# Kernel optimization log

Measured on AMD Instinct MI355X. Metric: run time of the kernel, lower is better.

## Reference

```python
import jax, jax.numpy as jnp
import numpy as np

B, NA, T, NV, D = 24, 50, 10, 196, 512


def setup_inputs() -> dict:
    key = jax.random.key(0)
    k1, k2 = jax.random.split(key)
    return {
        "audio_feats": jax.random.normal(k1, (B, NA, D), dtype=jnp.float32),
        "visual_feats": jax.random.normal(k2, (B, T, NV, D), dtype=jnp.float32),
        "temperature": jnp.float32(2.5),
        "scale_factor": jnp.float32(2.5),
        "threshold": jnp.float32(-2.5),
    }


def _l2norm(x):
    # F.normalize(dim=-1): x / max(||x||, 1e-12)
    n = jnp.sqrt(jnp.sum(x * x, axis=-1, keepdims=True))
    return x / jnp.maximum(n, 1e-12)


def reference(audio_feats, visual_feats, temperature, scale_factor, threshold):
    b = audio_feats.shape[0]
    a = _l2norm(audio_feats)          # (B,Na,D)
    v = _l2norm(visual_feats)         # (B,T,Nv,D)
    # all-pairs token similarities: (B,B,Na,T,Nv)
    sims = jnp.einsum('xad,ytvd->xyatv', a, v) / temperature

    # aggregate_temporal_similarities
    th = jax.nn.sigmoid(threshold)
    max_vis = jnp.max(sims, axis=-1)            # (B,B,Na,T)
    raw_diff = max_vis - th
    sel = jax.nn.relu(raw_diff) * scale_factor  # selection strength
    weighted_sum = jnp.sum(max_vis * sel, axis=-1)   # over T
    weights_sum = jnp.sum(sel, axis=-1)
    token_sims = weighted_sum / jnp.maximum(weights_sum, 1e-6)
    clip_sims = jnp.mean(token_sims, axis=-1)   # (B,B)
    fraction_selected = jnp.mean((raw_diff > 0).astype(jnp.float32))

    # InfoNCE
    idx = jnp.arange(b)
    losses_a2v = -jax.nn.log_softmax(clip_sims, axis=1)[idx, idx]
    losses_v2a = -jax.nn.log_softmax(clip_sims.T, axis=1)[idx, idx]
    contrastive_loss = jnp.mean(losses_a2v + losses_v2a) / 2

    # regularization
    neg = jnp.clip(sims, -20.0, 0.0)
    l_nonneg = jnp.mean(neg * neg)
    temp_low = jnp.maximum(-jnp.log(temperature), 0.0) ** 2   # log(1)=0
    temp_high = jnp.maximum(jnp.log(temperature) - jnp.log(4.0), 0.0) ** 2
    l_cal = temp_low + temp_high
    l_threshold = jnp.maximum(th - 0.9, 0.0) ** 2 + jnp.maximum(0.1 - th, 0.0) ** 2
    l_scale = jnp.maximum(scale_factor - 20.0, 0.0) ** 2 + jnp.maximum(1.0 - scale_factor, 0.0) ** 2
    reg_loss = 0.15 * l_nonneg + 2.0 * l_cal + 0.1 * l_threshold + 0.1 * l_scale

    # selection reward on positive pairs (diagonal)
    pos_diffs = raw_diff[idx, idx]                       # (B,Na,T)
    sel_ratio = (jnp.tanh(20.0 * pos_diffs) + 1.0) / 2.0
    selection_reward = -0.1 * jnp.log1p(jnp.mean(sel_ratio))

    total_loss = selection_reward + contrastive_loss + reg_loss
    return (total_loss, contrastive_loss, reg_loss, fraction_selected, selection_reward)
```

## Files before the change

kernel.cpp:

```cpp
#include <hip/hip_runtime.h>
#include <math.h>

#define B_   24
#define NA_  50
#define T_   10
#define NV_  196
#define D_   512
#define M_   1200
#define MPAD 1280
#define NVP  224
#define YT_  240
#define VROWS (YT_ * NVP)
#define ABLK 320

typedef __bf16 bf16x8 __attribute__((ext_vector_type(8)));
typedef float  f32x4  __attribute__((ext_vector_type(4)));
typedef unsigned short ushort8 __attribute__((ext_vector_type(8)));

__device__ __forceinline__ unsigned short f2bf(float f) {
    unsigned u = __float_as_uint(f);
    u += 0x7FFF + ((u >> 16) & 1);
    return (unsigned short)(u >> 16);
}

__device__ __forceinline__ void gload16(const void* g, void* l) {
    __builtin_amdgcn_global_load_lds(
        (const __attribute__((address_space(1))) unsigned int*)g,
        (__attribute__((address_space(3))) unsigned int*)l, 16, 0, 0);
}

__global__ void normconv_kernel(const float* __restrict__ a,
                                const float* __restrict__ vf,
                                const float* __restrict__ tempPtr,
                                unsigned short* __restrict__ Abf,
                                unsigned short* __restrict__ Vbf,
                                float* __restrict__ accs) {
    if (blockIdx.x == 0 && threadIdx.x < 4) accs[threadIdx.x] = 0.0f;
    int w = threadIdx.x >> 6, lane = threadIdx.x & 63;
    int bid = blockIdx.x;
    const float* src = nullptr;
    ushort8* dst;
    float tscale = 1.0f;
    if (bid < ABLK) {
        int row = bid * 4 + w;
        dst = (ushort8*)(Abf + (size_t)row * D_ + lane * 8);
        if (row < M_) { src = a + (size_t)row * D_ + lane * 8; tscale = tempPtr[0]; }
    } else {
        int row = (bid - ABLK) * 4 + w;
        dst = (ushort8*)(Vbf + (size_t)row * D_ + lane * 8);
        int yt = row / NVP, vv = row - yt * NVP;
        if (vv < NV_) src = vf + ((size_t)yt * NV_ + vv) * D_ + lane * 8;
    }
    if (src) {
        float4 u = *(const float4*)src;
        float4 v = *(const float4*)(src + 4);
        float s = u.x*u.x + u.y*u.y + u.z*u.z + u.w*u.w
                + v.x*v.x + v.y*v.y + v.z*v.z + v.w*v.w;
        #pragma unroll
        for (int off = 32; off; off >>= 1) s += __shfl_xor(s, off, 64);
        float sc = 1.0f / (fmaxf(sqrtf(s), 1e-12f) * tscale);
        ushort8 o;
        o[0]=f2bf(u.x*sc); o[1]=f2bf(u.y*sc); o[2]=f2bf(u.z*sc); o[3]=f2bf(u.w*sc);
        o[4]=f2bf(v.x*sc); o[5]=f2bf(v.y*sc); o[6]=f2bf(v.z*sc); o[7]=f2bf(v.w*sc);
        *dst = o;
    } else {
        ushort8 z = (ushort8)0;
        *dst = z;
    }
}

__global__ __launch_bounds__(256) void simred_kernel(
    const unsigned short* __restrict__ Abf, const unsigned short* __restrict__ Vbf,
    float* __restrict__ maxvis, float* __restrict__ accNonneg)
{
    __shared__ __align__(16) unsigned char lds[8192 + 14336];
    __shared__ float maxred[2][128];
    __shared__ float redbuf[4];

    const int tid  = threadIdx.x;
    const int lane = tid & 63;
    const int w    = tid >> 6;
    const int lrow = lane >> 2;
    const int lcol = lane & 3;
    const int q    = lane >> 4;
    const int m16  = lane & 15;
    const int wr   = w & 1;
    const int wc   = w >> 1;

    const int lin = blockIdx.y * gridDim.x + blockIdx.x;
    const int swz = (lin & 7) * 300 + (lin >> 3);
    const int bx  = swz % 10;
    const int yt  = swz / 10;
    const int rowA0 = bx * 128;
    const size_t vRow0 = (size_t)yt * NVP;

    const int scol = lcol ^ ((lrow >> 1) & 3);
    const unsigned short* gp[6];
    const unsigned char*  lp[6];
    int nun = 0;
    for (int u = w; u < 22; u += 4) {
        if (u < 8) gp[nun] = Abf + ((size_t)(rowA0 + u * 16 + lrow)) * D_ + scol * 8;
        else       gp[nun] = Vbf + (vRow0 + (size_t)((u - 8) * 16 + lrow)) * D_ + scol * 8;
        lp[nun] = lds + u * 1024;
        ++nun;
    }

    const unsigned rsw = (unsigned)((m16 >> 1) & 3) * 16u;
    unsigned aoff[4], boff[7];
    #pragma unroll
    for (int i = 0; i < 4; ++i)
        aoff[i] = (unsigned)(wr * 64 + i * 16 + m16) * 64u + (((unsigned)q * 16u) ^ rsw);
    #pragma unroll
    for (int j = 0; j < 7; ++j)
        boff[j] = 8192u + (unsigned)(wc * 112 + j * 16 + m16) * 64u + (((unsigned)q * 16u) ^ rsw);

    f32x4 acc[4][7];
    #pragma unroll
    for (int i = 0; i < 4; ++i)
        #pragma unroll
        for (int j = 0; j < 7; ++j) acc[i][j] = (f32x4)0.0f;

    #pragma unroll 6
    for (int i = 0; i < 6; ++i)
        if (i < nun) gload16(gp[i], (void*)lp[i]);
    __syncthreads();

    for (int c = 0; c < 16; ++c) {
        bf16x8 af[4], bfr[7];
        #pragma unroll
        for (int i = 0; i < 4; ++i) af[i] = *(const bf16x8*)(lds + aoff[i]);
        #pragma unroll
        for (int j = 0; j < 7; ++j) bfr[j] = *(const bf16x8*)(lds + boff[j]);
        __syncthreads();
        if (c < 15) {
            const int kc2 = (c + 1) * 32;
            #pragma unroll 6
            for (int i = 0; i < 6; ++i)
                if (i < nun) gload16(gp[i] + kc2, (void*)lp[i]);
        }
        #pragma unroll
        for (int i = 0; i < 4; ++i)
            #pragma unroll
            for (int j = 0; j < 7; ++j)
                acc[i][j] = __builtin_amdgcn_mfma_f32_16x16x32_bf16(af[i], bfr[j], acc[i][j], 0, 0, 0);
        __syncthreads();
    }

    float cs = 0.0f;
    #pragma unroll
    for (int i = 0; i < 4; ++i)
        #pragma unroll
        for (int j = 0; j < 7; ++j)
            #pragma unroll
            for (int r = 0; r < 4; ++r) {
                float v = acc[i][j][r];
                float cv = fminf(fmaxf(v, -20.0f), 0.0f);
                cs += cv * cv;
            }
    #pragma unroll
    for (int off = 32; off; off >>= 1) cs += __shfl_xor(cs, off, 64);
    if (lane == 0) redbuf[w] = cs;

    bool colv[7];
    #pragma unroll
    for (int j = 0; j < 7; ++j) colv[j] = (wc * 112 + j * 16 + m16) < NV_;
    #pragma unroll
    for (int i = 0; i < 4; ++i) {
        float mx[4] = {-3e38f, -3e38f, -3e38f, -3e38f};
        #pragma unroll
        for (int j = 0; j < 7; ++j)
            #pragma unroll
            for (int r = 0; r < 4; ++r)
                mx[r] = fmaxf(mx[r], colv[j] ? acc[i][j][r] : -3e38f);
        #pragma unroll
        for (int r = 0; r < 4; ++r) {
            float mm = mx[r];
            #pragma unroll
            for (int off = 1; off <= 8; off <<= 1) mm = fmaxf(mm, __shfl_xor(mm, off, 64));
            if (m16 == 0) maxred[wc][wr * 64 + i * 16 + q * 4 + r] = mm;
        }
    }
    __syncthreads();
    if (tid == 0) atomicAdd(accNonneg, redbuf[0] + redbuf[1] + redbuf[2] + redbuf[3]);
    if (tid < 128) {
        float mm = fmaxf(maxred[0][tid], maxred[1][tid]);
        int R = rowA0 + tid;
        if (R < M_) {
            int x = R / NA_, a = R - x * NA_;
            int y = yt / T_, t = yt - y * T_;
            maxvis[(((size_t)x * B_ + y) * NA_ + a) * T_ + t] = mm;
        }
    }
}

__global__ void aggfin_kernel(const float* __restrict__ maxvis,
                              const float* __restrict__ thrPtr,
                              const float* __restrict__ scalePtr,
                              const float* __restrict__ tempPtr,
                              float* __restrict__ clipSims,
                              float* __restrict__ accs,
                              float* __restrict__ out)
{
    int xy = blockIdx.x;
    int x = xy / B_, y = xy % B_;
    int a = threadIdx.x;
    float th    = 1.0f / (1.0f + expf(-thrPtr[0]));
    float scale = scalePtr[0];
    float token = 0.0f, cnt = 0.0f, selsum = 0.0f;
    if (a < NA_) {
        const float* p = maxvis + (((size_t)x * B_ + y) * NA_ + a) * T_;
        float ws = 0.0f, ss = 0.0f;
        #pragma unroll
        for (int t = 0; t < T_; ++t) {
            float mv  = p[t];
            float rd  = mv - th;
            float sel = fmaxf(rd, 0.0f) * scale;
            ws += mv * sel;
            ss += sel;
            if (rd > 0.0f) cnt += 1.0f;
            if (x == y) selsum += 0.5f * (tanhf(20.0f * rd) + 1.0f);
        }
        token = ws / fmaxf(ss, 1e-6f);
    }
    #pragma unroll
    for (int off = 32; off; off >>= 1) {
        token  += __shfl_xor(token,  off, 64);
        cnt    += __shfl_xor(cnt,    off, 64);
        selsum += __shfl_xor(selsum, off, 64);
    }
    if (threadIdx.x == 0) {
        clipSims[x * B_ + y] = token / (float)NA_;
        atomicAdd(&accs[1], cnt);
        if (x == y) atomicAdd(&accs[2], selsum);
    }
    __threadfence();
    unsigned last = 0;
    if (threadIdx.x == 0) {
        unsigned v = atomicAdd((unsigned int*)(accs + 3), 1u);
        last = ((v % (unsigned)(B_ * B_)) == (unsigned)(B_ * B_ - 1));
    }
    last = __shfl((int)last, 0, 64);
    if (!last) return;
    __threadfence();

    __shared__ float cs[B_ * B_];
    int tid = threadIdx.x;
    for (int i = tid; i < B_ * B_; i += 64) cs[i] = clipSims[i];
    __syncthreads();
    float lsum = 0.0f;
    if (tid < B_) {
        int i = tid;
        float m = -1e30f;
        for (int j = 0; j < B_; ++j) m = fmaxf(m, cs[i * B_ + j]);
        float e = 0.0f;
        for (int j = 0; j < B_; ++j) e += expf(cs[i * B_ + j] - m);
        float la = m + logf(e) - cs[i * B_ + i];
        float m2 = -1e30f;
        for (int j = 0; j < B_; ++j) m2 = fmaxf(m2, cs[j * B_ + i]);
        float e2 = 0.0f;
        for (int j = 0; j < B_; ++j) e2 += expf(cs[j * B_ + i] - m2);
        float lv = m2 + logf(e2) - cs[i * B_ + i];
        lsum = la + lv;
    }
    #pragma unroll
    for (int off = 32; off; off >>= 1) lsum += __shfl_xor(lsum, off, 64);
    if (tid == 0) {
        float contrastive = lsum / (float)B_ * 0.5f;
        float temp = tempPtr[0], scl = scalePtr[0];
        float l_nonneg = accs[0] / 56448000.0f;
        float logt = logf(temp);
        float tl  = fmaxf(-logt, 0.0f);
        float thi = fmaxf(logt - logf(4.0f), 0.0f);
        float l_cal = tl * tl + thi * thi;
        float t1 = fmaxf(th - 0.9f, 0.0f), t2 = fmaxf(0.1f - th, 0.0f);
        float l_thr = t1 * t1 + t2 * t2;
        float s1 = fmaxf(scl - 20.0f, 0.0f), s2 = fmaxf(1.0f - scl, 0.0f);
        float l_scale = s1 * s1 + s2 * s2;
        float reg = 0.15f * l_nonneg + 2.0f * l_cal + 0.1f * l_thr + 0.1f * l_scale;
        float frac   = accs[1] / 288000.0f;
        float selrew = -0.1f * log1pf(accs[2] / 12000.0f);
        out[0] = selrew + contrastive + reg;
        out[1] = contrastive;
        out[2] = reg;
        out[3] = frac;
        out[4] = selrew;
    }
}

extern "C" void kernel_launch(void* const* d_in, const int* in_sizes, int n_in,
                              void* d_out, int out_size, void* d_ws, size_t ws_size,
                              hipStream_t stream) {
    const float* audio  = (const float*)d_in[0];
    const float* visual = (const float*)d_in[1];
    const float* temp   = (const float*)d_in[2];
    const float* scale  = (const float*)d_in[3];
    const float* thr    = (const float*)d_in[4];
    float* out = (float*)d_out;

    unsigned char* wsb = (unsigned char*)d_ws;
    unsigned short* Abf = (unsigned short*)wsb;
    unsigned short* Vbf = (unsigned short*)(wsb + 1310720);
    float* maxvis   = (float*)(wsb + 1310720 + 55050240);
    float* clipSims = (float*)(wsb + 1310720 + 55050240 + 1152000);
    float* accs     = clipSims + 576;

    normconv_kernel<<<ABLK + VROWS / 4, 256, 0, stream>>>(audio, visual, temp, Abf, Vbf, accs);

    dim3 grid(MPAD / 128, YT_);
    simred_kernel<<<grid, 256, 0, stream>>>(Abf, Vbf, maxvis, accs);

    aggfin_kernel<<<B_ * B_, 64, 0, stream>>>(maxvis, thr, scale, temp, clipSims, accs, out);
}
```

Before: 285.9 us.

## Load MFMA operands directly from global memory instead of staging through LDS

Removes the LDS staging buffer and the global_load_lds double-step, so each wave reads its bf16 A and V fragments straight from global memory (via cache) inside a fully unrolled K loop, with no barriers. It also sets launch bounds to allow two blocks per CU. This trades the LDS writes and reads and the per-iteration syncs for redundant global/L2 traffic, since fragments shared across waves are now fetched separately by each wave. The operands also lose cooperative coalesced loading.

Result: slower. 408.7 us (+42.9%).

```diff
diff --git a/kernel.cpp b/kernel.cpp
--- a/kernel.cpp
+++ b/kernel.cpp
@@ -21,12 +21,6 @@
     unsigned u = __float_as_uint(f);
     u += 0x7FFF + ((u >> 16) & 1);
     return (unsigned short)(u >> 16);
-}
-
-__device__ __forceinline__ void gload16(const void* g, void* l) {
-    __builtin_amdgcn_global_load_lds(
-        (const __attribute__((address_space(1))) unsigned int*)g,
-        (__attribute__((address_space(3))) unsigned int*)l, 16, 0, 0);
 }
 
 __global__ void normconv_kernel(const float* __restrict__ a,
@@ -69,19 +63,16 @@
     }
 }
 
-__global__ __launch_bounds__(256) void simred_kernel(
+__global__ __launch_bounds__(256, 2) void simred_kernel(
     const unsigned short* __restrict__ Abf, const unsigned short* __restrict__ Vbf,
     float* __restrict__ maxvis, float* __restrict__ accNonneg)
 {
-    __shared__ __align__(16) unsigned char lds[8192 + 14336];
     __shared__ float maxred[2][128];
     __shared__ float redbuf[4];
 
     const int tid  = threadIdx.x;
     const int lane = tid & 63;
     const int w    = tid >> 6;
-    const int lrow = lane >> 2;
-    const int lcol = lane & 3;
     const int q    = lane >> 4;
     const int m16  = lane & 15;
     const int wr   = w & 1;
@@ -94,25 +85,14 @@
     const int rowA0 = bx * 128;
     const size_t vRow0 = (size_t)yt * NVP;
 
-    const int scol = lcol ^ ((lrow >> 1) & 3);
-    const unsigned short* gp[6];
-    const unsigned char*  lp[6];
-    int nun = 0;
-    for (int u = w; u < 22; u += 4) {
-        if (u < 8) gp[nun] = Abf + ((size_t)(rowA0 + u * 16 + lrow)) * D_ + scol * 8;
-        else       gp[nun] = Vbf + (vRow0 + (size_t)((u - 8) * 16 + lrow)) * D_ + scol * 8;
-        lp[nun] = lds + u * 1024;
-        ++nun;
-    }
-
-    const unsigned rsw = (unsigned)((m16 >> 1) & 3) * 16u;
-    unsigned aoff[4], boff[7];
+    const unsigned short* pA[4];
+    const unsigned short* pB[7];
     #pragma unroll
     for (int i = 0; i < 4; ++i)
-        aoff[i] = (unsigned)(wr * 64 + i * 16 + m16) * 64u + (((unsigned)q * 16u) ^ rsw);
+        pA[i] = Abf + ((size_t)(rowA0 + wr * 64 + i * 16 + m16)) * D_ + q * 8;
     #pragma unroll
     for (int j = 0; j < 7; ++j)
-        boff[j] = 8192u + (unsigned)(wc * 112 + j * 16 + m16) * 64u + (((unsigned)q * 16u) ^ rsw);
+        pB[j] = Vbf + (vRow0 + (size_t)(wc * 112 + j * 16 + m16)) * D_ + q * 8;
 
     f32x4 acc[4][7];
     #pragma unroll
@@ -120,30 +100,18 @@
         #pragma unroll
         for (int j = 0; j < 7; ++j) acc[i][j] = (f32x4)0.0f;
 
-    #pragma unroll 6
-    for (int i = 0; i < 6; ++i)
-        if (i < nun) gload16(gp[i], (void*)lp[i]);
-    __syncthreads();
-
+    #pragma unroll
     for (int c = 0; c < 16; ++c) {
-        bf16x8 af[4], bfr[7];
-        #pragma unroll
-        for (int i = 0; i < 4; ++i) af[i] = *(const bf16x8*)(lds + aoff[i]);
-        #pragma unroll
-        for (int j = 0; j < 7; ++j) bfr[j] = *(const bf16x8*)(lds + boff[j]);
-        __syncthreads();
-        if (c < 15) {
-            const int kc2 = (c + 1) * 32;
-            #pragma unroll 6
-            for (int i = 0; i < 6; ++i)
-                if (i < nun) gload16(gp[i] + kc2, (void*)lp[i]);
-        }
+        bf16x8 af[4], bv[7];
+        #pragma unroll
+        for (int i = 0; i < 4; ++i) af[i] = *(const bf16x8*)(pA[i] + c * 32);
+        #pragma unroll
+        for (int j = 0; j < 7; ++j) bv[j] = *(const bf16x8*)(pB[j] + c * 32);
         #pragma unroll
         for (int i = 0; i < 4; ++i)
             #pragma unroll
             for (int j = 0; j < 7; ++j)
-                acc[i][j] = __builtin_amdgcn_mfma_f32_16x16x32_bf16(af[i], bfr[j], acc[i][j], 0, 0, 0);
-        __syncthreads();
+                acc[i][j] = __builtin_amdgcn_mfma_f32_16x16x32_bf16(af[i], bv[j], acc[i][j], 0, 0, 0);
     }
 
     float cs = 0.0f;
```
